# Optimization experiments

Measured on AMD Instinct MI355X. Metric: run time of the kernel, lower is better.

The kernel has to match this reference:

```python
import jax, jax.numpy as jnp
import numpy as np

EMBED_DIM = 256
NUM_HEADS = 8
PROJ_DIM = EMBED_DIM // NUM_HEADS


def setup_inputs() -> dict:
    key = jax.random.key(0)
    ks = jax.random.split(key, 5)
    scale = 1.0 / np.sqrt(EMBED_DIM)
    inputs = jax.random.normal(ks[0], (2, 12, 12, 12, EMBED_DIM), dtype=jnp.float32)
    Wq = jax.random.normal(ks[1], (EMBED_DIM, EMBED_DIM), dtype=jnp.float32) * scale
    Wk = jax.random.normal(ks[2], (EMBED_DIM, EMBED_DIM), dtype=jnp.float32) * scale
    Wv = jax.random.normal(ks[3], (EMBED_DIM, EMBED_DIM), dtype=jnp.float32) * scale
    Wo = jax.random.normal(ks[4], (EMBED_DIM, EMBED_DIM), dtype=jnp.float32) * scale
    z = jnp.zeros((EMBED_DIM,), dtype=jnp.float32)
    return {"inputs": inputs, "Wq": Wq, "bq": z, "Wk": Wk, "bk": z,
            "Wv": Wv, "bv": z, "Wo": Wo, "bo": z}


def reference(inputs, Wq, bq, Wk, bk, Wv, bv, Wo, bo):
    B, h, w, d, E = inputs.shape
    S = h * w * d  # flattened spatial sequence
    x = inputs.reshape(B, S, E)
    # projections + head split: [B, S, E] -> [B, H, S, P]
    def split_heads(t):
        return t.reshape(B, S, NUM_HEADS, PROJ_DIM).transpose(0, 2, 1, 3)
    q = split_heads(x @ Wq + bq)
    k = split_heads(x @ Wk + bk)
    v = split_heads(x @ Wv + bv)
    # NOTE: original module does NOT scale by 1/sqrt(proj_dim)
    scores = jnp.einsum('bhsp,bhtp->bhst', q, k)  # [B, H, S, S]
    attn = jax.nn.softmax(scores, axis=-1)
    out = jnp.einsum('bhst,bhtp->bhsp', attn, v)  # [B, H, S, P]
    out = out.transpose(0, 2, 1, 3).reshape(B, h, w, d, E)
    return out @ Wo + bo
```

## Files before the change

### kernel.cpp

```cpp
#include <hip/hip_runtime.h>
#include <math.h>

#define EMBED 256
#define HEADS 8
#define PDIM  32
#define BATCH 2
#define SEQ   1728
#define NTOK  (BATCH*SEQ)
#define NE    (NTOK*EMBED)
#define LOG2E 1.44269504088896f

typedef __attribute__((ext_vector_type(8))) __bf16 bf16x8;
typedef __attribute__((ext_vector_type(4))) float  f32x4;
typedef unsigned short ushort_t;
typedef unsigned int   uint_t;

static __device__ __forceinline__ unsigned short f2bf_rne(float f) {
    union { float f; unsigned u; } x; x.f = f;
    unsigned r = x.u + 0x7fffu + ((x.u >> 16) & 1u);
    return (unsigned short)(r >> 16);
}
union v8cast { uint4 u; bf16x8 v; };

static __device__ __forceinline__ void cvt8_hilo(const float f[8], bf16x8& hi, bf16x8& lo) {
    uint4 ph, pl;
    uint_t* phv = (uint_t*)&ph; uint_t* plv = (uint_t*)&pl;
    #pragma unroll
    for (int j = 0; j < 4; ++j) {
        const float f0 = f[2 * j], f1 = f[2 * j + 1];
        const uint_t u0 = __float_as_uint(f0) + 0x8000u;
        const uint_t u1 = __float_as_uint(f1) + 0x8000u;
        phv[j] = __builtin_amdgcn_perm(u1, u0, 0x07060302u);
        const float l0 = f0 - __uint_as_float(u0 & 0xFFFF0000u);
        const float l1 = f1 - __uint_as_float(u1 & 0xFFFF0000u);
        plv[j] = __builtin_amdgcn_perm(__float_as_uint(l1) + 0x8000u,
                                       __float_as_uint(l0) + 0x8000u, 0x07060302u);
    }
    v8cast ch; ch.u = ph; hi = ch.v;
    v8cast cl; cl.u = pl; lo = cl.v;
}

__global__ __launch_bounds__(64) void qkv_gemm_kernel(
    const float* __restrict__ x,
    const float* __restrict__ Wq, const float* __restrict__ bq,
    const float* __restrict__ Wk, const float* __restrict__ bk,
    const float* __restrict__ Wv, const float* __restrict__ bv,
    ushort_t* __restrict__ qo, ushort_t* __restrict__ ko, ushort_t* __restrict__ vt)
{
    const int lane = threadIdx.x, li = lane & 15, quad = lane >> 4;
    const int m0 = blockIdx.x * 16, n0 = blockIdx.y * 32, z = blockIdx.z;
    const float* __restrict__ W    = (z == 0) ? Wq : (z == 1) ? Wk : Wv;
    const float* __restrict__ bias = (z == 0) ? bq : (z == 1) ? bk : bv;

    const float* ap = x + (size_t)(m0 + li) * EMBED + quad * 8;

    f32x4 acc[2];
    acc[0] = (f32x4){0.f, 0.f, 0.f, 0.f};
    acc[1] = (f32x4){0.f, 0.f, 0.f, 0.f};

    #pragma unroll
    for (int k0 = 0; k0 < EMBED; k0 += 32) {
        float af[8];
        *(float4*)&af[0] = *(const float4*)(ap + k0);
        *(float4*)&af[4] = *(const float4*)(ap + k0 + 4);
        bf16x8 ah, al;
        cvt8_hilo(af, ah, al);

        bf16x8 bh[2], bl[2];
        #pragma unroll
        for (int nt = 0; nt < 2; ++nt) {
            const int n = n0 + nt * 16 + li;
            const float* wp = W + (size_t)(k0 + quad * 8) * EMBED + n;
            float bf[8];
            #pragma unroll
            for (int jj = 0; jj < 8; ++jj) bf[jj] = wp[(size_t)jj * EMBED];
            cvt8_hilo(bf, bh[nt], bl[nt]);
        }
        #pragma unroll
        for (int nt = 0; nt < 2; ++nt) {
            acc[nt] = __builtin_amdgcn_mfma_f32_16x16x32_bf16(ah, bh[nt], acc[nt], 0, 0, 0);
            acc[nt] = __builtin_amdgcn_mfma_f32_16x16x32_bf16(al, bh[nt], acc[nt], 0, 0, 0);
            acc[nt] = __builtin_amdgcn_mfma_f32_16x16x32_bf16(ah, bl[nt], acc[nt], 0, 0, 0);
        }
    }

    const int b = m0 / SEQ;
    const int sbase = m0 - b * SEQ;

    if (z <= 1) {
        ushort_t* __restrict__ dst = z ? ko : qo;
        #pragma unroll
        for (int nt = 0; nt < 2; ++nt) {
            const int gcol = n0 + nt * 16 + li;
            const int h = gcol >> 5, p = gcol & 31;
            const float bb = bias[gcol];
            ushort_t* base = dst + ((size_t)(b * HEADS + h) * SEQ) * PDIM + p;
            #pragma unroll
            for (int r = 0; r < 4; ++r) {
                const int s = sbase + quad * 4 + r;
                base[(size_t)s * PDIM] = f2bf_rne(acc[nt][r] + bb);
            }
        }
    } else {
        #pragma unroll
        for (int nt = 0; nt < 2; ++nt) {
            const int gcol = n0 + nt * 16 + li;
            const int h = gcol >> 5, p = gcol & 31;
            const float bb = bias[gcol];
            ushort_t* base = vt + ((size_t)(b * HEADS + h) * PDIM + p) * SEQ;
            const int s0 = sbase + quad * 4;
            ushort4 w;
            w.x = f2bf_rne(acc[nt][0] + bb);
            w.y = f2bf_rne(acc[nt][1] + bb);
            w.z = f2bf_rne(acc[nt][2] + bb);
            w.w = f2bf_rne(acc[nt][3] + bb);
            *(ushort4*)&base[s0] = w;
        }
    }
}

__global__ __launch_bounds__(256) void attn_kernel(
    const ushort_t* __restrict__ q, const ushort_t* __restrict__ k,
    const ushort_t* __restrict__ vt, ushort_t* __restrict__ aob)
{
    const int t    = threadIdx.x;
    const int lane = t & 63;
    const int li   = lane & 15;
    const int quad = lane >> 4;
    const int w    = t >> 6;
    const int pr   = w >> 1;
    const int c    = w & 1;
    const int bh = blockIdx.y;
    const int b  = bh >> 3, h = bh & 7;
    const int q0 = (blockIdx.x * 2 + pr) * 16;

    const ushort_t* __restrict__ qb = q  + (size_t)bh * SEQ * PDIM;
    const ushort_t* __restrict__ kb = k  + (size_t)bh * SEQ * PDIM;
    const ushort_t* __restrict__ vb = vt + (size_t)bh * PDIM * SEQ;

    __shared__ ushort_t Ps[4][16][72];
    __shared__ float OS[2][16][32];
    __shared__ float mS[2][16], lS[2][16];

    const bf16x8 qfrag = *(const bf16x8*)(qb + (size_t)(q0 + li) * PDIM + quad * 8);

    const ushort_t* kptr = kb + (size_t)li * PDIM + quad * 8;
    const ushort_t* vptr = vb + (size_t)li * SEQ + quad * 8;

    f32x4 o0 = {0.f, 0.f, 0.f, 0.f};
    f32x4 o1 = {0.f, 0.f, 0.f, 0.f};
    float m_run = -__builtin_inff(), l_run = 0.f;

    bf16x8 kf0[4], vf0[4], kf1[4], vf1[4];

#define LOAD_TILE(KF, VF, J0) do {                                           \
        const ushort_t* kp = kptr + (size_t)(J0) * PDIM;                     \
        KF[0] = *(const bf16x8*)(kp);                                        \
        KF[1] = *(const bf16x8*)(kp + 16 * PDIM);                            \
        KF[2] = *(const bf16x8*)(kp + 32 * PDIM);                            \
        KF[3] = *(const bf16x8*)(kp + 48 * PDIM);                            \
        const ushort_t* vp = vptr + (J0);                                    \
        VF[0] = *(const bf16x8*)(vp);                                        \
        VF[1] = *(const bf16x8*)(vp + 16 * SEQ);                             \
        VF[2] = *(const bf16x8*)(vp + 32);                                   \
        VF[3] = *(const bf16x8*)(vp + 32 + 16 * SEQ);                        \
    } while (0)

    auto compute_tile = [&](const bf16x8* kf, const bf16x8* vf) {
        const f32x4 zero = {0.f, 0.f, 0.f, 0.f};
        f32x4 st[4];
        #pragma unroll
        for (int jt = 0; jt < 4; ++jt)
            st[jt] = __builtin_amdgcn_mfma_f32_16x16x32_bf16(kf[jt], qfrag, zero, 0, 0, 0);

        float tm = st[0][0];
        #pragma unroll
        for (int jt = 0; jt < 4; ++jt)
            #pragma unroll
            for (int r = 0; r < 4; ++r) tm = fmaxf(tm, st[jt][r]);
        tm = fmaxf(tm, __shfl_xor(tm, 16));
        tm = fmaxf(tm, __shfl_xor(tm, 32));
        const float mnew  = fmaxf(m_run, tm);
        const float negml = -(mnew * LOG2E);

        float ps = 0.f;
        #pragma unroll
        for (int jt = 0; jt < 4; ++jt) {
            const float p0 = __builtin_amdgcn_exp2f(fmaf(st[jt][0], LOG2E, negml));
            const float p1 = __builtin_amdgcn_exp2f(fmaf(st[jt][1], LOG2E, negml));
            const float p2 = __builtin_amdgcn_exp2f(fmaf(st[jt][2], LOG2E, negml));
            const float p3 = __builtin_amdgcn_exp2f(fmaf(st[jt][3], LOG2E, negml));
            ps += (p0 + p1) + (p2 + p3);
            uint2 pw;
            pw.x = __builtin_amdgcn_perm(__float_as_uint(p1) + 0x8000u,
                                         __float_as_uint(p0) + 0x8000u, 0x07060302u);
            pw.y = __builtin_amdgcn_perm(__float_as_uint(p3) + 0x8000u,
                                         __float_as_uint(p2) + 0x8000u, 0x07060302u);
            *(uint2*)&Ps[w][li][16 * jt + 4 * quad] = pw;
        }
        ps += __shfl_xor(ps, 16);
        ps += __shfl_xor(ps, 32);

        const float alpha = __builtin_amdgcn_exp2f(fmaf(m_run, LOG2E, negml));
        l_run = fmaf(l_run, alpha, ps);
        m_run = mnew;

        float af[4];
        #pragma unroll
        for (int r = 0; r < 4; ++r) af[r] = __shfl(alpha, 4 * quad + r);
        #pragma unroll
        for (int r = 0; r < 4; ++r) { o0[r] *= af[r]; o1[r] *= af[r]; }

        const bf16x8 pa0 = *(const bf16x8*)&Ps[w][li][8 * quad];
        const bf16x8 pa1 = *(const bf16x8*)&Ps[w][li][32 + 8 * quad];
        o0 = __builtin_amdgcn_mfma_f32_16x16x32_bf16(pa0, vf[0], o0, 0, 0, 0);
        o0 = __builtin_amdgcn_mfma_f32_16x16x32_bf16(pa1, vf[2], o0, 0, 0, 0);
        o1 = __builtin_amdgcn_mfma_f32_16x16x32_bf16(pa0, vf[1], o1, 0, 0, 0);
        o1 = __builtin_amdgcn_mfma_f32_16x16x32_bf16(pa1, vf[3], o1, 0, 0, 0);
    };

    const int jstart = c ? 896 : 0;
    const int ntl    = c ? 13 : 14;

    LOAD_TILE(kf0, vf0, jstart);
    for (int kt = 0; kt < ntl; kt += 2) {
        if (kt + 1 < ntl) LOAD_TILE(kf1, vf1, jstart + (kt + 1) * 64);
        compute_tile(kf0, vf0);
        if (kt + 1 < ntl) {
            if (kt + 2 < ntl) LOAD_TILE(kf0, vf0, jstart + (kt + 2) * 64);
            compute_tile(kf1, vf1);
        }
    }
#undef LOAD_TILE

    if (c == 1) {
        if (quad == 0) { mS[pr][li] = m_run; lS[pr][li] = l_run; }
        #pragma unroll
        for (int r = 0; r < 4; ++r) {
            OS[pr][4 * quad + r][li]      = o0[r];
            OS[pr][4 * quad + r][16 + li] = o1[r];
        }
    }
    __syncthreads();
    if (c == 0) {
        const float m1 = mS[pr][li], l1 = lS[pr][li];
        const float M  = fmaxf(m_run, m1);
        const float a0 = __builtin_amdgcn_exp2f((m_run - M) * LOG2E);
        const float a1 = __builtin_amdgcn_exp2f((m1    - M) * LOG2E);
        const float lt = a0 * l_run + a1 * l1;
        #pragma unroll
        for (int r = 0; r < 4; ++r) {
            const int row = 4 * quad + r;
            const float af0  = __shfl(a0, row);
            const float af1  = __shfl(a1, row);
            const float linv = 1.0f / __shfl(lt, row);
            const float v0 = (af0 * o0[r] + af1 * OS[pr][row][li])      * linv;
            const float v1 = (af0 * o1[r] + af1 * OS[pr][row][16 + li]) * linv;
            const int s = q0 + row;
            ushort_t* orow = aob + ((size_t)(b * SEQ + s)) * EMBED + h * PDIM;
            orow[li]      = f2bf_rne(v0);
            orow[16 + li] = f2bf_rne(v1);
        }
    }
}

__global__ __launch_bounds__(64) void out_gemm_kernel(
    const ushort_t* __restrict__ a, const float* __restrict__ Wo,
    const float* __restrict__ bo, float* __restrict__ out)
{
    const int lane = threadIdx.x, li = lane & 15, quad = lane >> 4;
    const int m0 = blockIdx.x * 16, n0 = blockIdx.y * 16;

    const ushort_t* aph = a + (size_t)(m0 + li) * EMBED + quad * 8;

    f32x4 acc = {0.f, 0.f, 0.f, 0.f};

    #pragma unroll
    for (int k0 = 0; k0 < EMBED; k0 += 32) {
        const bf16x8 ah = *(const bf16x8*)(aph + k0);
        const float* wp = Wo + (size_t)(k0 + quad * 8) * EMBED + n0 + li;
        uint4 pb;
        uint_t* pbv = (uint_t*)&pb;
        #pragma unroll
        for (int j = 0; j < 4; ++j) {
            const uint_t u0 = __float_as_uint(wp[(size_t)(2 * j) * EMBED])     + 0x8000u;
            const uint_t u1 = __float_as_uint(wp[(size_t)(2 * j + 1) * EMBED]) + 0x8000u;
            pbv[j] = __builtin_amdgcn_perm(u1, u0, 0x07060302u);
        }
        v8cast cb; cb.u = pb;
        acc = __builtin_amdgcn_mfma_f32_16x16x32_bf16(ah, cb.v, acc, 0, 0, 0);
    }

    const float bb = bo[n0 + li];
    #pragma unroll
    for (int r = 0; r < 4; ++r) {
        const int row = m0 + 4 * quad + r;
        out[(size_t)row * EMBED + n0 + li] = acc[r] + bb;
    }
}

extern "C" void kernel_launch(void* const* d_in, const int* in_sizes, int n_in,
                              void* d_out, int out_size, void* d_ws, size_t ws_size,
                              hipStream_t stream)
{
    const float* x  = (const float*)d_in[0];
    const float* Wq = (const float*)d_in[1];
    const float* bq = (const float*)d_in[2];
    const float* Wk = (const float*)d_in[3];
    const float* bk = (const float*)d_in[4];
    const float* Wv = (const float*)d_in[5];
    const float* bv = (const float*)d_in[6];
    const float* Wo = (const float*)d_in[7];
    const float* bo = (const float*)d_in[8];
    float* out = (float*)d_out;

    ushort_t* ws  = (ushort_t*)d_ws;
    ushort_t* qb  = ws;
    ushort_t* kb  = qb + (size_t)NE;
    ushort_t* vt  = kb + (size_t)NE;
    ushort_t* aob = vt + (size_t)NE;

    qkv_gemm_kernel<<<dim3(NTOK / 16, 8, 3), 64, 0, stream>>>(
        x, Wq, bq, Wk, bk, Wv, bv, qb, kb, vt);
    attn_kernel<<<dim3(SEQ / 32, BATCH * HEADS), 256, 0, stream>>>(qb, kb, vt, aob);
    out_gemm_kernel<<<dim3(NTOK / 16, 16), 64, 0, stream>>>(aob, Wo, bo, out);
}
```

Baseline: 136.5 us.

## Share K/V tiles via LDS in attention and widen GEMM row tiles

The attention kernel no longer splits the key range between pairs of waves and merges their partial results. Instead, four waves each own 16 queries and cooperatively stage each 64-key K and V tile into double-buffered shared memory, with a register prefetch of the next tile, so each K/V tile is read from global once per block rather than once per wave. The QKV and output GEMM kernels now compute 64 rows per block instead of 16, reusing each converted weight fragment across four M tiles. The trade-off is a __syncthreads per key tile, half as many attention blocks, more registers in the GEMMs, and fewer GEMM blocks in flight.

Result: faster. 121.5 us (-11.0%).

```diff
diff --git a/kernel.cpp b/kernel.cpp
--- a/kernel.cpp
+++ b/kernel.cpp
@@ -8,6 +8,7 @@
 #define SEQ   1728
 #define NTOK  (BATCH*SEQ)
 #define NE    (NTOK*EMBED)
+#define NKT   (SEQ/64)
 #define LOG2E 1.44269504088896f
 
 typedef __attribute__((ext_vector_type(8))) __bf16 bf16x8;
@@ -48,24 +49,29 @@
     ushort_t* __restrict__ qo, ushort_t* __restrict__ ko, ushort_t* __restrict__ vt)
 {
     const int lane = threadIdx.x, li = lane & 15, quad = lane >> 4;
-    const int m0 = blockIdx.x * 16, n0 = blockIdx.y * 32, z = blockIdx.z;
+    const int m0 = blockIdx.x * 64, n0 = blockIdx.y * 32, z = blockIdx.z;
     const float* __restrict__ W    = (z == 0) ? Wq : (z == 1) ? Wk : Wv;
     const float* __restrict__ bias = (z == 0) ? bq : (z == 1) ? bk : bv;
 
     const float* ap = x + (size_t)(m0 + li) * EMBED + quad * 8;
 
-    f32x4 acc[2];
-    acc[0] = (f32x4){0.f, 0.f, 0.f, 0.f};
-    acc[1] = (f32x4){0.f, 0.f, 0.f, 0.f};
-
-    #pragma unroll
+    f32x4 acc[4][2];
+    #pragma unroll
+    for (int mt = 0; mt < 4; ++mt)
+        #pragma unroll
+        for (int nt = 0; nt < 2; ++nt)
+            acc[mt][nt] = (f32x4){0.f, 0.f, 0.f, 0.f};
+
+    #pragma unroll 2
     for (int k0 = 0; k0 < EMBED; k0 += 32) {
-        float af[8];
-        *(float4*)&af[0] = *(const float4*)(ap + k0);
-        *(float4*)&af[4] = *(const float4*)(ap + k0 + 4);
-        bf16x8 ah, al;
-        cvt8_hilo(af, ah, al);
-
+        bf16x8 ah[4], al[4];
+        #pragma unroll
+        for (int mt = 0; mt < 4; ++mt) {
+            float af[8];
+            *(float4*)&af[0] = *(const float4*)(ap + (size_t)mt * 16 * EMBED + k0);
+            *(float4*)&af[4] = *(const float4*)(ap + (size_t)mt * 16 * EMBED + k0 + 4);
+            cvt8_hilo(af, ah[mt], al[mt]);
+        }
         bf16x8 bh[2], bl[2];
         #pragma unroll
         for (int nt = 0; nt < 2; ++nt) {
@@ -77,11 +83,13 @@
             cvt8_hilo(bf, bh[nt], bl[nt]);
         }
         #pragma unroll
-        for (int nt = 0; nt < 2; ++nt) {
-            acc[nt] = __builtin_amdgcn_mfma_f32_16x16x32_bf16(ah, bh[nt], acc[nt], 0, 0, 0);
-            acc[nt] = __builtin_amdgcn_mfma_f32_16x16x32_bf16(al, bh[nt], acc[nt], 0, 0, 0);
-            acc[nt] = __builtin_amdgcn_mfma_f32_16x16x32_bf16(ah, bl[nt], acc[nt], 0, 0, 0);
-        }
+        for (int mt = 0; mt < 4; ++mt)
+            #pragma unroll
+            for (int nt = 0; nt < 2; ++nt) {
+                acc[mt][nt] = __builtin_amdgcn_mfma_f32_16x16x32_bf16(ah[mt], bh[nt], acc[mt][nt], 0, 0, 0);
+                acc[mt][nt] = __builtin_amdgcn_mfma_f32_16x16x32_bf16(al[mt], bh[nt], acc[mt][nt], 0, 0, 0);
+                acc[mt][nt] = __builtin_amdgcn_mfma_f32_16x16x32_bf16(ah[mt], bl[nt], acc[mt][nt], 0, 0, 0);
+            }
     }
 
     const int b = m0 / SEQ;
@@ -96,10 +104,12 @@
             const float bb = bias[gcol];
             ushort_t* base = dst + ((size_t)(b * HEADS + h) * SEQ) * PDIM + p;
             #pragma unroll
-            for (int r = 0; r < 4; ++r) {
-                const int s = sbase + quad * 4 + r;
-                base[(size_t)s * PDIM] = f2bf_rne(acc[nt][r] + bb);
-            }
+            for (int mt = 0; mt < 4; ++mt)
+                #pragma unroll
+                for (int r = 0; r < 4; ++r) {
+                    const int s = sbase + mt * 16 + quad * 4 + r;
+                    base[(size_t)s * PDIM] = f2bf_rne(acc[mt][nt][r] + bb);
+                }
         }
     } else {
         #pragma unroll
@@ -108,13 +118,16 @@
             const int h = gcol >> 5, p = gcol & 31;
             const float bb = bias[gcol];
             ushort_t* base = vt + ((size_t)(b * HEADS + h) * PDIM + p) * SEQ;
-            const int s0 = sbase + quad * 4;
-            ushort4 w;
-            w.x = f2bf_rne(acc[nt][0] + bb);
-            w.y = f2bf_rne(acc[nt][1] + bb);
-            w.z = f2bf_rne(acc[nt][2] + bb);
-            w.w = f2bf_rne(acc[nt][3] + bb);
-            *(ushort4*)&base[s0] = w;
+            #pragma unroll
+            for (int mt = 0; mt < 4; ++mt) {
+                const int s0 = sbase + mt * 16 + quad * 4;
+                ushort4 w;
+                w.x = f2bf_rne(acc[mt][nt][0] + bb);
+                w.y = f2bf_rne(acc[mt][nt][1] + bb);
+                w.z = f2bf_rne(acc[mt][nt][2] + bb);
+                w.w = f2bf_rne(acc[mt][nt][3] + bb);
+                *(ushort4*)&base[s0] = w;
+            }
         }
     }
 }
@@ -125,53 +138,52 @@
 {
     const int t    = threadIdx.x;
     const int lane = t & 63;
+    const int w    = t >> 6;
     const int li   = lane & 15;
     const int quad = lane >> 4;
-    const int w    = t >> 6;
-    const int pr   = w >> 1;
-    const int c    = w & 1;
     const int bh = blockIdx.y;
     const int b  = bh >> 3, h = bh & 7;
-    const int q0 = (blockIdx.x * 2 + pr) * 16;
+    const int q0 = blockIdx.x * 64 + w * 16;
 
     const ushort_t* __restrict__ qb = q  + (size_t)bh * SEQ * PDIM;
     const ushort_t* __restrict__ kb = k  + (size_t)bh * SEQ * PDIM;
     const ushort_t* __restrict__ vb = vt + (size_t)bh * PDIM * SEQ;
 
+    __shared__ ushort_t Ks[2][64][40];
+    __shared__ ushort_t Vs[2][32][72];
     __shared__ ushort_t Ps[4][16][72];
-    __shared__ float OS[2][16][32];
-    __shared__ float mS[2][16], lS[2][16];
 
     const bf16x8 qfrag = *(const bf16x8*)(qb + (size_t)(q0 + li) * PDIM + quad * 8);
 
-    const ushort_t* kptr = kb + (size_t)li * PDIM + quad * 8;
-    const ushort_t* vptr = vb + (size_t)li * SEQ + quad * 8;
+    const int jk = w * 16 + (lane >> 2), ck = (lane & 3) * 8;
+    const int pv = w * 8 + (lane >> 3),  cv = (lane & 7) * 8;
+    const ushort_t* kgp = kb + (size_t)jk * PDIM + ck;
+    const ushort_t* vgp = vb + (size_t)pv * SEQ + cv;
 
     f32x4 o0 = {0.f, 0.f, 0.f, 0.f};
     f32x4 o1 = {0.f, 0.f, 0.f, 0.f};
     float m_run = -__builtin_inff(), l_run = 0.f;
 
-    bf16x8 kf0[4], vf0[4], kf1[4], vf1[4];
-
-#define LOAD_TILE(KF, VF, J0) do {                                           \
-        const ushort_t* kp = kptr + (size_t)(J0) * PDIM;                     \
-        KF[0] = *(const bf16x8*)(kp);                                        \
-        KF[1] = *(const bf16x8*)(kp + 16 * PDIM);                            \
-        KF[2] = *(const bf16x8*)(kp + 32 * PDIM);                            \
-        KF[3] = *(const bf16x8*)(kp + 48 * PDIM);                            \
-        const ushort_t* vp = vptr + (J0);                                    \
-        VF[0] = *(const bf16x8*)(vp);                                        \
-        VF[1] = *(const bf16x8*)(vp + 16 * SEQ);                             \
-        VF[2] = *(const bf16x8*)(vp + 32);                                   \
-        VF[3] = *(const bf16x8*)(vp + 32 + 16 * SEQ);                        \
-    } while (0)
-
-    auto compute_tile = [&](const bf16x8* kf, const bf16x8* vf) {
+    uint4 kreg = *(const uint4*)(kgp);
+    uint4 vreg = *(const uint4*)(vgp);
+
+    for (int kt = 0; kt < NKT; ++kt) {
+        const int p = kt & 1;
+        *(uint4*)&Ks[p][jk][ck] = kreg;
+        *(uint4*)&Vs[p][pv][cv] = vreg;
+        __syncthreads();
+        if (kt + 1 < NKT) {
+            kreg = *(const uint4*)(kgp + (size_t)(kt + 1) * 64 * PDIM);
+            vreg = *(const uint4*)(vgp + (kt + 1) * 64);
+        }
+
         const f32x4 zero = {0.f, 0.f, 0.f, 0.f};
         f32x4 st[4];
         #pragma unroll
-        for (int jt = 0; jt < 4; ++jt)
-            st[jt] = __builtin_amdgcn_mfma_f32_16x16x32_bf16(kf[jt], qfrag, zero, 0, 0, 0);
+        for (int jt = 0; jt < 4; ++jt) {
+            const bf16x8 kf = *(const bf16x8*)&Ks[p][jt * 16 + li][quad * 8];
+            st[jt] = __builtin_amdgcn_mfma_f32_16x16x32_bf16(kf, qfrag, zero, 0, 0, 0);
+        }
 
         float tm = st[0][0];
         #pragma unroll
@@ -213,54 +225,25 @@
 
         const bf16x8 pa0 = *(const bf16x8*)&Ps[w][li][8 * quad];
         const bf16x8 pa1 = *(const bf16x8*)&Ps[w][li][32 + 8 * quad];
-        o0 = __builtin_amdgcn_mfma_f32_16x16x32_bf16(pa0, vf[0], o0, 0, 0, 0);
-        o0 = __builtin_amdgcn_mfma_f32_16x16x32_bf16(pa1, vf[2], o0, 0, 0, 0);
-        o1 = __builtin_amdgcn_mfma_f32_16x16x32_bf16(pa0, vf[1], o1, 0, 0, 0);
-        o1 = __builtin_amdgcn_mfma_f32_16x16x32_bf16(pa1, vf[3], o1, 0, 0, 0);
-    };
-
-    const int jstart = c ? 896 : 0;
-    const int ntl    = c ? 13 : 14;
-
-    LOAD_TILE(kf0, vf0, jstart);
-    for (int kt = 0; kt < ntl; kt += 2) {
-        if (kt + 1 < ntl) LOAD_TILE(kf1, vf1, jstart + (kt + 1) * 64);
-        compute_tile(kf0, vf0);
-        if (kt + 1 < ntl) {
-            if (kt + 2 < ntl) LOAD_TILE(kf0, vf0, jstart + (kt + 2) * 64);
-            compute_tile(kf1, vf1);
-        }
-    }
-#undef LOAD_TILE
-
-    if (c == 1) {
-        if (quad == 0) { mS[pr][li] = m_run; lS[pr][li] = l_run; }
-        #pragma unroll
-        for (int r = 0; r < 4; ++r) {
-            OS[pr][4 * quad + r][li]      = o0[r];
-            OS[pr][4 * quad + r][16 + li] = o1[r];
-        }
-    }
-    __syncthreads();
-    if (c == 0) {
-        const float m1 = mS[pr][li], l1 = lS[pr][li];
-        const float M  = fmaxf(m_run, m1);
-        const float a0 = __builtin_amdgcn_exp2f((m_run - M) * LOG2E);
-        const float a1 = __builtin_amdgcn_exp2f((m1    - M) * LOG2E);
-        const float lt = a0 * l_run + a1 * l1;
-        #pragma unroll
-        for (int r = 0; r < 4; ++r) {
-            const int row = 4 * quad + r;
-            const float af0  = __shfl(a0, row);
-            const float af1  = __shfl(a1, row);
-            const float linv = 1.0f / __shfl(lt, row);
-            const float v0 = (af0 * o0[r] + af1 * OS[pr][row][li])      * linv;
-            const float v1 = (af0 * o1[r] + af1 * OS[pr][row][16 + li]) * linv;
-            const int s = q0 + row;
-            ushort_t* orow = aob + ((size_t)(b * SEQ + s)) * EMBED + h * PDIM;
-            orow[li]      = f2bf_rne(v0);
-            orow[16 + li] = f2bf_rne(v1);
-        }
+        const bf16x8 vf00 = *(const bf16x8*)&Vs[p][li][quad * 8];
+        const bf16x8 vf01 = *(const bf16x8*)&Vs[p][16 + li][quad * 8];
+        const bf16x8 vf10 = *(const bf16x8*)&Vs[p][li][32 + quad * 8];
+        const bf16x8 vf11 = *(const bf16x8*)&Vs[p][16 + li][32 + quad * 8];
+        o0 = __builtin_amdgcn_mfma_f32_16x16x32_bf16(pa0, vf00, o0, 0, 0, 0);
+        o0 = __builtin_amdgcn_mfma_f32_16x16x32_bf16(pa1, vf10, o0, 0, 0, 0);
+        o1 = __builtin_amdgcn_mfma_f32_16x16x32_bf16(pa0, vf01, o1, 0, 0, 0);
+        o1 = __builtin_amdgcn_mfma_f32_16x16x32_bf16(pa1, vf11, o1, 0, 0, 0);
+    }
+
+    float linv[4];
+    #pragma unroll
+    for (int r = 0; r < 4; ++r) linv[r] = 1.0f / __shfl(l_run, 4 * quad + r);
+    #pragma unroll
+    for (int r = 0; r < 4; ++r) {
+        const int s = q0 + 4 * quad + r;
+        ushort_t* row = aob + ((size_t)(b * SEQ + s)) * EMBED + h * PDIM;
+        row[li]      = f2bf_rne(o0[r] * linv[r]);
+        row[16 + li] = f2bf_rne(o1[r] * linv[r]);
     }
 }
 
@@ -269,15 +252,20 @@
     const float* __restrict__ bo, float* __restrict__ out)
 {
     const int lane = threadIdx.x, li = lane & 15, quad = lane >> 4;
-    const int m0 = blockIdx.x * 16, n0 = blockIdx.y * 16;
+    const int m0 = blockIdx.x * 64, n0 = blockIdx.y * 16;
 
     const ushort_t* aph = a + (size_t)(m0 + li) * EMBED + quad * 8;
 
-    f32x4 acc = {0.f, 0.f, 0.f, 0.f};
-
-    #pragma unroll
+    f32x4 acc[4];
+    #pragma unroll
+    for (int mt = 0; mt < 4; ++mt) acc[mt] = (f32x4){0.f, 0.f, 0.f, 0.f};
+
+    #pragma unroll 2
     for (int k0 = 0; k0 < EMBED; k0 += 32) {
-        const bf16x8 ah = *(const bf16x8*)(aph + k0);
+        bf16x8 ah[4];
+        #pragma unroll
+        for (int mt = 0; mt < 4; ++mt)
+            ah[mt] = *(const bf16x8*)(aph + (size_t)mt * 16 * EMBED + k0);
         const float* wp = Wo + (size_t)(k0 + quad * 8) * EMBED + n0 + li;
         uint4 pb;
         uint_t* pbv = (uint_t*)&pb;
@@ -288,15 +276,19 @@
             pbv[j] = __builtin_amdgcn_perm(u1, u0, 0x07060302u);
         }
         v8cast cb; cb.u = pb;
-        acc = __builtin_amdgcn_mfma_f32_16x16x32_bf16(ah, cb.v, acc, 0, 0, 0);
+        #pragma unroll
+        for (int mt = 0; mt < 4; ++mt)
+            acc[mt] = __builtin_amdgcn_mfma_f32_16x16x32_bf16(ah[mt], cb.v, acc[mt], 0, 0, 0);
     }
 
     const float bb = bo[n0 + li];
     #pragma unroll
-    for (int r = 0; r < 4; ++r) {
-        const int row = m0 + 4 * quad + r;
-        out[(size_t)row * EMBED + n0 + li] = acc[r] + bb;
-    }
+    for (int mt = 0; mt < 4; ++mt)
+        #pragma unroll
+        for (int r = 0; r < 4; ++r) {
+            const int row = m0 + mt * 16 + quad * 4 + r;
+            out[(size_t)row * EMBED + n0 + li] = acc[mt][r] + bb;
+        }
 }
 
 extern "C" void kernel_launch(void* const* d_in, const int* in_sizes, int n_in,
@@ -320,8 +312,8 @@
     ushort_t* vt  = kb + (size_t)NE;
     ushort_t* aob = vt + (size_t)NE;
 
-    qkv_gemm_kernel<<<dim3(NTOK / 16, 8, 3), 64, 0, stream>>>(
+    qkv_gemm_kernel<<<dim3(NTOK / 64, 8, 3), 64, 0, stream>>>(
         x, Wq, bq, Wk, bk, Wv, bv, qb, kb, vt);
-    attn_kernel<<<dim3(SEQ / 32, BATCH * HEADS), 256, 0, stream>>>(qb, kb, vt, aob);
-    out_gemm_kernel<<<dim3(NTOK / 16, 16), 64, 0, stream>>>(aob, Wo, bo, out);
-}
+    attn_kernel<<<dim3(SEQ / 64, BATCH * HEADS), 256, 0, stream>>>(qb, kb, vt, aob);
+    out_gemm_kernel<<<dim3(NTOK / 64, 16), 64, 0, stream>>>(aob, Wo, bo, out);
+}
```
